# Optimization experiments

Hardware: AMD Instinct MI355X
Metric: run time of the kernel (lower is better)

Reference implementation:

```python
import jax, jax.numpy as jnp
import numpy as np
from jax import lax

# Topology constants (windowed DAG: compute node i, at global index N_IN+i,
# reads the FANIN immediately preceding global node values).
N_IN = 16      # number of input nodes
FANIN = 16     # connections per compute node
N_NODES = 512  # topologically ordered compute nodes (hidden + output)
N_OUT = 64     # last N_OUT nodes in node_order are outputs
BATCH = 32768
T = N_IN + N_NODES  # total node count


def setup_inputs() -> dict:
    key = jax.random.key(0)
    k1, k2, k3, k4 = jax.random.split(key, 4)
    x = jax.random.normal(k1, (BATCH, N_IN), dtype=jnp.float32)
    # weights scaled down so tanh is not fully saturated through 512 layers
    weights = jax.random.normal(k2, (N_NODES, FANIN), dtype=jnp.float32) * 0.25
    biases = jax.random.normal(k3, (N_NODES,), dtype=jnp.float32) * 0.1
    responses = 1.0 + 0.1 * jax.random.normal(k4, (N_NODES,), dtype=jnp.float32)
    # src indices for node i: global indices [i, i+FANIN) (== previous FANIN nodes,
    # since N_IN == FANIN). Shape [N_NODES, FANIN], int32, all in [0, T).
    src_idx = (jnp.arange(N_NODES, dtype=jnp.int32)[:, None]
               + jnp.arange(FANIN, dtype=jnp.int32)[None, :]
               + (N_IN - FANIN))
    return {"x": x, "weights": weights, "biases": biases,
            "responses": responses, "src_idx": src_idx}


def _forward(x, weights, biases, responses, src_idx):
    B = x.shape[0]
    # values buffer [B, T]: inputs first, then compute nodes in topo order
    values0 = jnp.zeros((B, T), dtype=x.dtype).at[:, :N_IN].set(x)

    def body(values, xs):
        i, idx_row, w, b, r = xs
        src_vals = jnp.take(values, idx_row, axis=1)        # [B, FANIN] gather
        agg = src_vals @ w                                   # [B] weighted sum
        out = jnp.tanh(agg + b) * r                          # activation
        values = lax.dynamic_update_slice(values, out[:, None], (0, N_IN + i))
        return values, None

    ii = jnp.arange(N_NODES, dtype=jnp.int32)
    values, _ = lax.scan(body, values0, (ii, src_idx, weights, biases, responses))
    return values[:, T - N_OUT:]  # [B, N_OUT]


def reference(x, weights, biases, responses, src_idx):
    return _forward(x, weights, biases, responses, src_idx)
```

## Files before the change

kernel.cpp:

```cpp
#include <hip/hip_runtime.h>


typedef float v4f __attribute__((ext_vector_type(4)));
typedef float v2f __attribute__((ext_vector_type(2)));

constexpr int kNOut     = 64;
constexpr int kBatch    = 32768;
constexpr int kGStrideF = 48;
constexpr int kLdsFloats = (256 + 3) * kGStrideF;
constexpr float kScale  = 2.8853900817779268f;

#define QPERM(X, CTRL) __int_as_float(__builtin_amdgcn_update_dpp(            \
    __float_as_int(X), __float_as_int(X), (CTRL), 0xF, 0xF, false))

#define PREF(S) {                                                             \
    asm volatile(                                                             \
      "ds_read_b128 %0, %5 offset:0\n\t"                                      \
      "ds_read_b128 %1, %5 offset:16\n\t"                                     \
      "ds_read_b128 %2, %5 offset:64\n\t"                                     \
      "ds_read_b128 %3, %5 offset:80\n\t"                                     \
      "ds_read_b64  %4, %5 offset:128"                                        \
      : "=&v"(qa[S]), "=&v"(qb[S]), "=&v"(qc[S]), "=&v"(qd[S]), "=&v"(qm[S])  \
      : "v"(a));                                                              \
    a += kGStrideF * 4; }

#define WAITG(S)                                                              \
    asm volatile("s_waitcnt lgkmcnt(15)"                                      \
      : "+v"(qa[S]), "+v"(qb[S]), "+v"(qc[S]), "+v"(qd[S]), "+v"(qm[S]));

#define NODE1(WLO, WHI, BH, W0,W1,W2,W3,W4,W5,W6,W7) {                        \
    float p = fmaf((W0), (WLO).x, (BH));                                      \
    p = fmaf((W1), (WLO).y, p);                                               \
    p = fmaf((W2), (WLO).z, p);                                               \
    p = fmaf((W3), (WLO).w, p);                                               \
    p = fmaf((W4), (WHI).x, p);                                               \
    p = fmaf((W5), (WHI).y, p);                                               \
    p = fmaf((W6), (WHI).z, p);                                               \
    p = fmaf((W7), (WHI).w, p);                                               \
    float sf = p + QPERM(p, 0xB1);                   \
    float ex = __builtin_amdgcn_exp2f(sf);                                    \
    float un = __builtin_amdgcn_rcpf(ex + 1.0f);                              \
    float mg = QPERM((W0), 0xB1);                      \
    (W0) = is_l1 ? un : mg; }

#define GROUP(G, O0,O1,O2,O3,O4,O5,O6,O7, P0,P1,P2,P3,P4,P5,P6,P7) {          \
    PREF(((G) + 3) & 3)                                                       \
    WAITG((G) & 3)                                                            \
    NODE1(qa[(G) & 3], qb[(G) & 3], qm[(G) & 3].x,                            \
          O0,O1,O2,O3,O4,O5,O6,O7)                                            \
    NODE1(qc[(G) & 3], qd[(G) & 3], qm[(G) & 3].y,                            \
          P0,P1,P2,P3,P4,P5,P6,P7) }

__global__ __launch_bounds__(256) void neat_fwd(
    const float* __restrict__ x,
    const float* __restrict__ w,
    const float* __restrict__ bias,
    const float* __restrict__ resp,
    float* __restrict__ out)
{
    __shared__ alignas(16) float ldsw[kLdsFloats];
    __shared__ float rst[512];
    __shared__ float sums[512];

    const int t  = threadIdx.x;
    const int jl = t & 1;
    const bool is_l1 = (jl == 1);

    rst[t] = resp[t];
    rst[t + 256] = resp[t + 256];
    __syncthreads();

    const float4* __restrict__ w4 = reinterpret_cast<const float4*>(w);
    #pragma unroll
    for (int k = 0; k < 8; ++k) {
        int i4 = t + k * 256;
        float4 v = w4[i4];
        int n = i4 >> 2, k4 = i4 & 3;
        int s0 = n + 4 * k4;
        float rho0 = (s0 + 0 < 16) ? 1.0f : rst[s0 - 16];
        float rho1 = (s0 + 1 < 16) ? 1.0f : rst[s0 - 15];
        float rho2 = (s0 + 2 < 16) ? 1.0f : rst[s0 - 14];
        float rho3 = (s0 + 3 < 16) ? 1.0f : rst[s0 - 13];
        float wr0 = v.x * rho0, wr1 = v.y * rho1,
              wr2 = v.z * rho2, wr3 = v.w * rho3;
        float ps = (wr0 + wr1) + (wr2 + wr3);
        ps += QPERM(ps, 0xB1);
        ps += QPERM(ps, 0x4E);
        if ((t & 3) == 0) sums[n] = ps;
        const float m2k = -2.0f * kScale;
        float4 sc = make_float4(wr0 * m2k, wr1 * m2k, wr2 * m2k, wr3 * m2k);
        *reinterpret_cast<float4*>(
            &ldsw[(n >> 1) * kGStrideF + (n & 1) * 16 + k4 * 4]) = sc;
    }
    __syncthreads();

    #pragma unroll
    for (int k = 0; k < 2; ++k) {
        int n = t + k * 256;
        float Bh = (bias[n] + sums[n]) * (kScale * 0.5f);
        int q = n >> 1, s = n & 1;
        ldsw[q * kGStrideF + 32 + s] = Bh;
        ldsw[q * kGStrideF + 40 + s] = Bh;
    }

    const int e = blockIdx.x * 128 + (t >> 1);
    const float4 xa = reinterpret_cast<const float4*>(x)[e * 4 + 2 * jl];
    const float4 xb = reinterpret_cast<const float4*>(x)[e * 4 + 2 * jl + 1];
    float r0 = fmaf(-0.5f, xa.x, 0.5f);
    float r1 = fmaf(-0.5f, xa.y, 0.5f);
    float r2 = fmaf(-0.5f, xa.z, 0.5f);
    float r3 = fmaf(-0.5f, xa.w, 0.5f);
    float r4 = fmaf(-0.5f, xb.x, 0.5f);
    float r5 = fmaf(-0.5f, xb.y, 0.5f);
    float r6 = fmaf(-0.5f, xb.z, 0.5f);
    float r7 = fmaf(-0.5f, xb.w, 0.5f);

    const float4* __restrict__ rr4 = reinterpret_cast<const float4*>(resp);
    float* __restrict__ op = out + (size_t)e * kNOut + jl * 8;

    __syncthreads();

    unsigned int a = (unsigned int)(unsigned long long)(&ldsw[0])
                   + (unsigned int)(jl << 5);

    v4f qa[4], qb[4], qc[4], qd[4];
    v2f qm[4];
    PREF(0) PREF(1) PREF(2)

    #pragma unroll 1
    for (int g = 0; g < 32; ++g) {
        GROUP(0, r0,r1,r2,r3,r4,r5,r6,r7,  r1,r2,r3,r4,r5,r6,r7,r0)
        GROUP(1, r2,r3,r4,r5,r6,r7,r0,r1,  r3,r4,r5,r6,r7,r0,r1,r2)
        GROUP(2, r4,r5,r6,r7,r0,r1,r2,r3,  r5,r6,r7,r0,r1,r2,r3,r4)
        GROUP(3, r6,r7,r0,r1,r2,r3,r4,r5,  r7,r0,r1,r2,r3,r4,r5,r6)
        GROUP(4, r0,r1,r2,r3,r4,r5,r6,r7,  r1,r2,r3,r4,r5,r6,r7,r0)
        GROUP(5, r2,r3,r4,r5,r6,r7,r0,r1,  r3,r4,r5,r6,r7,r0,r1,r2)
        GROUP(6, r4,r5,r6,r7,r0,r1,r2,r3,  r5,r6,r7,r0,r1,r2,r3,r4)
        GROUP(7, r6,r7,r0,r1,r2,r3,r4,r5,  r7,r0,r1,r2,r3,r4,r5,r6)
        if (g >= 28) {
            int m = g - 28;
            const float4 ra = rr4[112 + 4 * m + 2 * jl];
            const float4 rb = rr4[112 + 4 * m + 2 * jl + 1];
            float4 o0 = make_float4(fmaf(-2.0f, r0, 1.0f) * ra.x,
                                    fmaf(-2.0f, r1, 1.0f) * ra.y,
                                    fmaf(-2.0f, r2, 1.0f) * ra.z,
                                    fmaf(-2.0f, r3, 1.0f) * ra.w);
            float4 o1 = make_float4(fmaf(-2.0f, r4, 1.0f) * rb.x,
                                    fmaf(-2.0f, r5, 1.0f) * rb.y,
                                    fmaf(-2.0f, r6, 1.0f) * rb.z,
                                    fmaf(-2.0f, r7, 1.0f) * rb.w);
            *reinterpret_cast<float4*>(op + 16 * m)     = o0;
            *reinterpret_cast<float4*>(op + 16 * m + 4) = o1;
        }
    }

    asm volatile("s_waitcnt lgkmcnt(0)" ::: "memory");
}

extern "C" void kernel_launch(void* const* d_in, const int* in_sizes, int n_in,
                              void* d_out, int out_size, void* d_ws, size_t ws_size,
                              hipStream_t stream) {
    const float* x    = (const float*)d_in[0];
    const float* w    = (const float*)d_in[1];
    const float* bias = (const float*)d_in[2];
    const float* resp = (const float*)d_in[3];
    float* out = (float*)d_out;
    dim3 block(256);
    dim3 grid(kBatch / 128);
    hipLaunchKernelGGL(neat_fwd, grid, block, 0, stream, x, w, bias, resp, out);
}
```

Before: 89.35 us.

## Process two batch elements per thread pair to reuse LDS weight reads

Each thread now carries two independent batch rows (A and B) through the 512-node chain, and the block shrinks from 256 to 128 threads while still covering 128 batch rows per block. Each LDS weight/bias read now feeds twice as many FMAs, halving LDS traffic per element. The two independent dependency chains also add ILP to hide exp/rcp and DPP latency. In exchange it uses more registers per thread and fewer waves per block, which may reduce occupancy-based latency hiding.

```diff
diff --git a/kernel.cpp b/kernel.cpp
--- a/kernel.cpp
+++ b/kernel.cpp
@@ -28,30 +28,39 @@
     asm volatile("s_waitcnt lgkmcnt(15)"                                      \
       : "+v"(qa[S]), "+v"(qb[S]), "+v"(qc[S]), "+v"(qd[S]), "+v"(qm[S]));
 
-#define NODE1(WLO, WHI, BH, W0,W1,W2,W3,W4,W5,W6,W7) {                        \
-    float p = fmaf((W0), (WLO).x, (BH));                                      \
-    p = fmaf((W1), (WLO).y, p);                                               \
-    p = fmaf((W2), (WLO).z, p);                                               \
-    p = fmaf((W3), (WLO).w, p);                                               \
-    p = fmaf((W4), (WHI).x, p);                                               \
-    p = fmaf((W5), (WHI).y, p);                                               \
-    p = fmaf((W6), (WHI).z, p);                                               \
-    p = fmaf((W7), (WHI).w, p);                                               \
-    float sf = p + QPERM(p, 0xB1);                   \
-    float ex = __builtin_amdgcn_exp2f(sf);                                    \
-    float un = __builtin_amdgcn_rcpf(ex + 1.0f);                              \
-    float mg = QPERM((W0), 0xB1);                      \
-    (W0) = is_l1 ? un : mg; }
+#define NODE1(WLO, WHI, BH, A0,A1,A2,A3,A4,A5,A6,A7,                          \
+                            B0,B1,B2,B3,B4,B5,B6,B7) {                        \
+    float pA = fmaf((A0), (WLO).x, (BH));                                     \
+    float pB = fmaf((B0), (WLO).x, (BH));                                     \
+    pA = fmaf((A1), (WLO).y, pA);  pB = fmaf((B1), (WLO).y, pB);              \
+    pA = fmaf((A2), (WLO).z, pA);  pB = fmaf((B2), (WLO).z, pB);              \
+    pA = fmaf((A3), (WLO).w, pA);  pB = fmaf((B3), (WLO).w, pB);              \
+    pA = fmaf((A4), (WHI).x, pA);  pB = fmaf((B4), (WHI).x, pB);              \
+    pA = fmaf((A5), (WHI).y, pA);  pB = fmaf((B5), (WHI).y, pB);              \
+    pA = fmaf((A6), (WHI).z, pA);  pB = fmaf((B6), (WHI).z, pB);              \
+    pA = fmaf((A7), (WHI).w, pA);  pB = fmaf((B7), (WHI).w, pB);              \
+    float sA = pA + QPERM(pA, 0xB1);                 \
+    float sB = pB + QPERM(pB, 0xB1);                                          \
+    float eA_ = __builtin_amdgcn_exp2f(sA);                                   \
+    float eB_ = __builtin_amdgcn_exp2f(sB);                                   \
+    float uA = __builtin_amdgcn_rcpf(eA_ + 1.0f);                             \
+    float uB = __builtin_amdgcn_rcpf(eB_ + 1.0f);                             \
+    float mA = QPERM((A0), 0xB1);                      \
+    float mB = QPERM((B0), 0xB1);                                             \
+    (A0) = is_l1 ? uA : mA;                                                   \
+    (B0) = is_l1 ? uB : mB; }
 
 #define GROUP(G, O0,O1,O2,O3,O4,O5,O6,O7, P0,P1,P2,P3,P4,P5,P6,P7) {          \
     PREF(((G) + 3) & 3)                                                       \
     WAITG((G) & 3)                                                            \
     NODE1(qa[(G) & 3], qb[(G) & 3], qm[(G) & 3].x,                            \
-          O0,O1,O2,O3,O4,O5,O6,O7)                                            \
+          rA##O0,rA##O1,rA##O2,rA##O3,rA##O4,rA##O5,rA##O6,rA##O7,            \
+          rB##O0,rB##O1,rB##O2,rB##O3,rB##O4,rB##O5,rB##O6,rB##O7)            \
     NODE1(qc[(G) & 3], qd[(G) & 3], qm[(G) & 3].y,                            \
-          P0,P1,P2,P3,P4,P5,P6,P7) }
+          rA##P0,rA##P1,rA##P2,rA##P3,rA##P4,rA##P5,rA##P6,rA##P7,            \
+          rB##P0,rB##P1,rB##P2,rB##P3,rB##P4,rB##P5,rB##P6,rB##P7) }
 
-__global__ __launch_bounds__(256) void neat_fwd(
+__global__ __launch_bounds__(128) void neat_fwd(
     const float* __restrict__ x,
     const float* __restrict__ w,
     const float* __restrict__ bias,
@@ -66,14 +75,14 @@
     const int jl = t & 1;
     const bool is_l1 = (jl == 1);
 
-    rst[t] = resp[t];
-    rst[t + 256] = resp[t + 256];
+    #pragma unroll
+    for (int k = 0; k < 4; ++k) rst[t + k * 128] = resp[t + k * 128];
     __syncthreads();
 
     const float4* __restrict__ w4 = reinterpret_cast<const float4*>(w);
     #pragma unroll
-    for (int k = 0; k < 8; ++k) {
-        int i4 = t + k * 256;
+    for (int k = 0; k < 16; ++k) {
+        int i4 = t + k * 128;
         float4 v = w4[i4];
         int n = i4 >> 2, k4 = i4 & 3;
         int s0 = n + 4 * k4;
@@ -95,28 +104,31 @@
     __syncthreads();
 
     #pragma unroll
-    for (int k = 0; k < 2; ++k) {
-        int n = t + k * 256;
+    for (int k = 0; k < 4; ++k) {
+        int n = t + k * 128;
         float Bh = (bias[n] + sums[n]) * (kScale * 0.5f);
         int q = n >> 1, s = n & 1;
         ldsw[q * kGStrideF + 32 + s] = Bh;
         ldsw[q * kGStrideF + 40 + s] = Bh;
     }
 
-    const int e = blockIdx.x * 128 + (t >> 1);
-    const float4 xa = reinterpret_cast<const float4*>(x)[e * 4 + 2 * jl];
-    const float4 xb = reinterpret_cast<const float4*>(x)[e * 4 + 2 * jl + 1];
-    float r0 = fmaf(-0.5f, xa.x, 0.5f);
-    float r1 = fmaf(-0.5f, xa.y, 0.5f);
-    float r2 = fmaf(-0.5f, xa.z, 0.5f);
-    float r3 = fmaf(-0.5f, xa.w, 0.5f);
-    float r4 = fmaf(-0.5f, xb.x, 0.5f);
-    float r5 = fmaf(-0.5f, xb.y, 0.5f);
-    float r6 = fmaf(-0.5f, xb.z, 0.5f);
-    float r7 = fmaf(-0.5f, xb.w, 0.5f);
+    const int eA = blockIdx.x * 128 + (t >> 1);
+    const int eB = eA + 64;
+    const float4* __restrict__ x4 = reinterpret_cast<const float4*>(x);
+    const float4 xa = x4[eA * 4 + 2 * jl], xb = x4[eA * 4 + 2 * jl + 1];
+    const float4 xc = x4[eB * 4 + 2 * jl], xd = x4[eB * 4 + 2 * jl + 1];
+    float rA0 = fmaf(-0.5f, xa.x, 0.5f), rA1 = fmaf(-0.5f, xa.y, 0.5f);
+    float rA2 = fmaf(-0.5f, xa.z, 0.5f), rA3 = fmaf(-0.5f, xa.w, 0.5f);
+    float rA4 = fmaf(-0.5f, xb.x, 0.5f), rA5 = fmaf(-0.5f, xb.y, 0.5f);
+    float rA6 = fmaf(-0.5f, xb.z, 0.5f), rA7 = fmaf(-0.5f, xb.w, 0.5f);
+    float rB0 = fmaf(-0.5f, xc.x, 0.5f), rB1 = fmaf(-0.5f, xc.y, 0.5f);
+    float rB2 = fmaf(-0.5f, xc.z, 0.5f), rB3 = fmaf(-0.5f, xc.w, 0.5f);
+    float rB4 = fmaf(-0.5f, xd.x, 0.5f), rB5 = fmaf(-0.5f, xd.y, 0.5f);
+    float rB6 = fmaf(-0.5f, xd.z, 0.5f), rB7 = fmaf(-0.5f, xd.w, 0.5f);
 
     const float4* __restrict__ rr4 = reinterpret_cast<const float4*>(resp);
-    float* __restrict__ op = out + (size_t)e * kNOut + jl * 8;
+    float* __restrict__ opA = out + (size_t)eA * kNOut + jl * 8;
+    float* __restrict__ opB = out + (size_t)eB * kNOut + jl * 8;
 
     __syncthreads();
 
@@ -129,28 +141,38 @@
 
     #pragma unroll 1
     for (int g = 0; g < 32; ++g) {
-        GROUP(0, r0,r1,r2,r3,r4,r5,r6,r7,  r1,r2,r3,r4,r5,r6,r7,r0)
-        GROUP(1, r2,r3,r4,r5,r6,r7,r0,r1,  r3,r4,r5,r6,r7,r0,r1,r2)
-        GROUP(2, r4,r5,r6,r7,r0,r1,r2,r3,  r5,r6,r7,r0,r1,r2,r3,r4)
-        GROUP(3, r6,r7,r0,r1,r2,r3,r4,r5,  r7,r0,r1,r2,r3,r4,r5,r6)
-        GROUP(4, r0,r1,r2,r3,r4,r5,r6,r7,  r1,r2,r3,r4,r5,r6,r7,r0)
-        GROUP(5, r2,r3,r4,r5,r6,r7,r0,r1,  r3,r4,r5,r6,r7,r0,r1,r2)
-        GROUP(6, r4,r5,r6,r7,r0,r1,r2,r3,  r5,r6,r7,r0,r1,r2,r3,r4)
-        GROUP(7, r6,r7,r0,r1,r2,r3,r4,r5,  r7,r0,r1,r2,r3,r4,r5,r6)
+        GROUP(0, 0,1,2,3,4,5,6,7,  1,2,3,4,5,6,7,0)
+        GROUP(1, 2,3,4,5,6,7,0,1,  3,4,5,6,7,0,1,2)
+        GROUP(2, 4,5,6,7,0,1,2,3,  5,6,7,0,1,2,3,4)
+        GROUP(3, 6,7,0,1,2,3,4,5,  7,0,1,2,3,4,5,6)
+        GROUP(4, 0,1,2,3,4,5,6,7,  1,2,3,4,5,6,7,0)
+        GROUP(5, 2,3,4,5,6,7,0,1,  3,4,5,6,7,0,1,2)
+        GROUP(6, 4,5,6,7,0,1,2,3,  5,6,7,0,1,2,3,4)
+        GROUP(7, 6,7,0,1,2,3,4,5,  7,0,1,2,3,4,5,6)
         if (g >= 28) {
             int m = g - 28;
             const float4 ra = rr4[112 + 4 * m + 2 * jl];
             const float4 rb = rr4[112 + 4 * m + 2 * jl + 1];
-            float4 o0 = make_float4(fmaf(-2.0f, r0, 1.0f) * ra.x,
-                                    fmaf(-2.0f, r1, 1.0f) * ra.y,
-                                    fmaf(-2.0f, r2, 1.0f) * ra.z,
-                                    fmaf(-2.0f, r3, 1.0f) * ra.w);
-            float4 o1 = make_float4(fmaf(-2.0f, r4, 1.0f) * rb.x,
-                                    fmaf(-2.0f, r5, 1.0f) * rb.y,
-                                    fmaf(-2.0f, r6, 1.0f) * rb.z,
-                                    fmaf(-2.0f, r7, 1.0f) * rb.w);
-            *reinterpret_cast<float4*>(op + 16 * m)     = o0;
-            *reinterpret_cast<float4*>(op + 16 * m + 4) = o1;
+            float4 oA0 = make_float4(fmaf(-2.0f, rA0, 1.0f) * ra.x,
+                                     fmaf(-2.0f, rA1, 1.0f) * ra.y,
+                                     fmaf(-2.0f, rA2, 1.0f) * ra.z,
+                                     fmaf(-2.0f, rA3, 1.0f) * ra.w);
+            float4 oA1 = make_float4(fmaf(-2.0f, rA4, 1.0f) * rb.x,
+                                     fmaf(-2.0f, rA5, 1.0f) * rb.y,
+                                     fmaf(-2.0f, rA6, 1.0f) * rb.z,
+                                     fmaf(-2.0f, rA7, 1.0f) * rb.w);
+            float4 oB0 = make_float4(fmaf(-2.0f, rB0, 1.0f) * ra.x,
+                                     fmaf(-2.0f, rB1, 1.0f) * ra.y,
+                                     fmaf(-2.0f, rB2, 1.0f) * ra.z,
+                                     fmaf(-2.0f, rB3, 1.0f) * ra.w);
+            float4 oB1 = make_float4(fmaf(-2.0f, rB4, 1.0f) * rb.x,
+                                     fmaf(-2.0f, rB5, 1.0f) * rb.y,
+                                     fmaf(-2.0f, rB6, 1.0f) * rb.z,
+                                     fmaf(-2.0f, rB7, 1.0f) * rb.w);
+            *reinterpret_cast<float4*>(opA + 16 * m)     = oA0;
+            *reinterpret_cast<float4*>(opA + 16 * m + 4) = oA1;
+            *reinterpret_cast<float4*>(opB + 16 * m)     = oB0;
+            *reinterpret_cast<float4*>(opB + 16 * m + 4) = oB1;
         }
     }
 
@@ -165,7 +187,7 @@
     const float* bias = (const float*)d_in[2];
     const float* resp = (const float*)d_in[3];
     float* out = (float*)d_out;
-    dim3 block(256);
+    dim3 block(128);
     dim3 grid(kBatch / 128);
     hipLaunchKernelGGL(neat_fwd, grid, block, 0, stream, x, w, bias, resp, out);
 }
```

Result: slower. 108.5 us (+21.4%).

## Shorten node dependency chain by splitting off the newest input term

Applied to the files above, without the earlier changes.

Reworks the per-node evaluation so the most recent predecessor's contribution (weight 15) is added after the cross-lane reduction. The other 15 terms can then be computed before the previous node finishes. Each lane pair now keeps an extra register (u0/u1) holding the latest result, and the lane data layout is shifted to match. This shortens the serial critical path through the 512-node chain. In exchange the LDS reads get wider, setup has more selects, and output staging is more complex.

```diff
diff --git a/kernel.cpp b/kernel.cpp
--- a/kernel.cpp
+++ b/kernel.cpp
@@ -2,7 +2,6 @@
 
 
 typedef float v4f __attribute__((ext_vector_type(4)));
-typedef float v2f __attribute__((ext_vector_type(2)));
 
 constexpr int kNOut     = 64;
 constexpr int kBatch    = 32768;
@@ -19,7 +18,7 @@
       "ds_read_b128 %1, %5 offset:16\n\t"                                     \
       "ds_read_b128 %2, %5 offset:64\n\t"                                     \
       "ds_read_b128 %3, %5 offset:80\n\t"                                     \
-      "ds_read_b64  %4, %5 offset:128"                                        \
+      "ds_read_b128 %4, %5 offset:128"                                        \
       : "=&v"(qa[S]), "=&v"(qb[S]), "=&v"(qc[S]), "=&v"(qd[S]), "=&v"(qm[S])  \
       : "v"(a));                                                              \
     a += kGStrideF * 4; }
@@ -28,28 +27,29 @@
     asm volatile("s_waitcnt lgkmcnt(15)"                                      \
       : "+v"(qa[S]), "+v"(qb[S]), "+v"(qc[S]), "+v"(qd[S]), "+v"(qm[S]));
 
-#define NODE1(WLO, WHI, BH, W0,W1,W2,W3,W4,W5,W6,W7) {                        \
-    float p = fmaf((W0), (WLO).x, (BH));                                      \
-    p = fmaf((W1), (WLO).y, p);                                               \
-    p = fmaf((W2), (WLO).z, p);                                               \
-    p = fmaf((W3), (WLO).w, p);                                               \
-    p = fmaf((W4), (WHI).x, p);                                               \
-    p = fmaf((W5), (WHI).y, p);                                               \
-    p = fmaf((W6), (WHI).z, p);                                               \
-    p = fmaf((W7), (WHI).w, p);                                               \
-    float sf = p + QPERM(p, 0xB1);                   \
-    float ex = __builtin_amdgcn_exp2f(sf);                                    \
-    float un = __builtin_amdgcn_rcpf(ex + 1.0f);                              \
-    float mg = QPERM((W0), 0xB1);                      \
-    (W0) = is_l1 ? un : mg; }
+#define NODE1(WLO, WHI, BH, W15, UIN, UOUT, A0,A1,A2,A3,A4,A5,A6,A7) {        \
+    float p = fmaf((A0), (WLO).x, (BH));                                      \
+    p = fmaf((A1), (WLO).y, p);                                               \
+    p = fmaf((A2), (WLO).z, p);                                               \
+    p = fmaf((A3), (WLO).w, p);                                               \
+    p = fmaf((A4), (WHI).x, p);                                               \
+    p = fmaf((A5), (WHI).y, p);                                               \
+    p = fmaf((A6), (WHI).z, p);                                               \
+    p = fmaf((A7), (WHI).w, p);                                               \
+    float s_ = p + QPERM(p, 0xB1);                   \
+    float mg = QPERM((A1), 0xB1);                      \
+    float acc = fmaf((UIN), (W15), s_);                \
+    float exv = __builtin_amdgcn_exp2f(acc);                                  \
+    (UOUT) = __builtin_amdgcn_rcpf(exv + 1.0f);                               \
+    (A0) = is_l1 ? (UIN) : mg; }
 
-#define GROUP(G, O0,O1,O2,O3,O4,O5,O6,O7, P0,P1,P2,P3,P4,P5,P6,P7) {          \
+#define GROUP(G, A0,A1,A2,A3,A4,A5,A6,A7) {                                   \
     PREF(((G) + 3) & 3)                                                       \
     WAITG((G) & 3)                                                            \
-    NODE1(qa[(G) & 3], qb[(G) & 3], qm[(G) & 3].x,                            \
-          O0,O1,O2,O3,O4,O5,O6,O7)                                            \
-    NODE1(qc[(G) & 3], qd[(G) & 3], qm[(G) & 3].y,                            \
-          P0,P1,P2,P3,P4,P5,P6,P7) }
+    NODE1(qa[(G)&3], qb[(G)&3], qm[(G)&3].x, qm[(G)&3].y, u0, u1,             \
+          A0,A1,A2,A3,A4,A5,A6,A7)                                            \
+    NODE1(qc[(G)&3], qd[(G)&3], qm[(G)&3].z, qm[(G)&3].w, u1, u0,             \
+          A1,A2,A3,A4,A5,A6,A7,A0) }
 
 __global__ __launch_bounds__(256) void neat_fwd(
     const float* __restrict__ x,
@@ -60,7 +60,6 @@
 {
     __shared__ alignas(16) float ldsw[kLdsFloats];
     __shared__ float rst[512];
-    __shared__ float sums[512];
 
     const int t  = threadIdx.x;
     const int jl = t & 1;
@@ -71,49 +70,54 @@
     __syncthreads();
 
     const float4* __restrict__ w4 = reinterpret_cast<const float4*>(w);
-    #pragma unroll
-    for (int k = 0; k < 8; ++k) {
-        int i4 = t + k * 256;
-        float4 v = w4[i4];
-        int n = i4 >> 2, k4 = i4 & 3;
-        int s0 = n + 4 * k4;
-        float rho0 = (s0 + 0 < 16) ? 1.0f : rst[s0 - 16];
-        float rho1 = (s0 + 1 < 16) ? 1.0f : rst[s0 - 15];
-        float rho2 = (s0 + 2 < 16) ? 1.0f : rst[s0 - 14];
-        float rho3 = (s0 + 3 < 16) ? 1.0f : rst[s0 - 13];
-        float wr0 = v.x * rho0, wr1 = v.y * rho1,
-              wr2 = v.z * rho2, wr3 = v.w * rho3;
-        float ps = (wr0 + wr1) + (wr2 + wr3);
-        ps += QPERM(ps, 0xB1);
-        ps += QPERM(ps, 0x4E);
-        if ((t & 3) == 0) sums[n] = ps;
-        const float m2k = -2.0f * kScale;
-        float4 sc = make_float4(wr0 * m2k, wr1 * m2k, wr2 * m2k, wr3 * m2k);
-        *reinterpret_cast<float4*>(
-            &ldsw[(n >> 1) * kGStrideF + (n & 1) * 16 + k4 * 4]) = sc;
-    }
-    __syncthreads();
-
+    const float m2k = -2.0f * kScale;
     #pragma unroll
     for (int k = 0; k < 2; ++k) {
-        int n = t + k * 256;
-        float Bh = (bias[n] + sums[n]) * (kScale * 0.5f);
-        int q = n >> 1, s = n & 1;
-        ldsw[q * kGStrideF + 32 + s] = Bh;
-        ldsw[q * kGStrideF + 40 + s] = Bh;
+        int n = t + (k << 8);
+        float4 a0 = w4[n*4+0], a1 = w4[n*4+1], a2 = w4[n*4+2], a3 = w4[n*4+3];
+        float wv0=a0.x, wv1=a0.y, wv2=a0.z, wv3=a0.w;
+        float wv4=a1.x, wv5=a1.y, wv6=a1.z, wv7=a1.w;
+        float wv8=a2.x, wv9=a2.y, wv10=a2.z, wv11=a2.w;
+        float wv12=a3.x, wv13=a3.y, wv14=a3.z, wv15=a3.w;
+        float sum = 0.0f;
+        float ws0,ws1,ws2,ws3,ws4,ws5,ws6,ws7,ws8,ws9,ws10,ws11,ws12,ws13,ws14,ws15;
+        #define DO(J) { float rho = (n + J < 16) ? 1.0f : rst[n + J - 16];    \
+                        float wr = wv##J * rho; sum += wr; ws##J = wr * m2k; }
+        DO(0) DO(1) DO(2) DO(3) DO(4) DO(5) DO(6) DO(7)
+        DO(8) DO(9) DO(10) DO(11) DO(12) DO(13) DO(14) DO(15)
+        #undef DO
+        int q = n >> 1, h = n & 1;
+        float* gb = ldsw + q * kGStrideF;
+        *reinterpret_cast<float4*>(gb + h*16 + 0)  = make_float4(ws0, ws1, ws2, ws3);
+        *reinterpret_cast<float4*>(gb + h*16 + 4)  = make_float4(ws4, ws5, ws6, ws7);
+        *reinterpret_cast<float4*>(gb + h*16 + 8)  = make_float4(0.0f, ws8, ws9, ws10);
+        *reinterpret_cast<float4*>(gb + h*16 + 12) = make_float4(ws11, ws12, ws13, ws14);
+        float Bh = (bias[n] + sum) * (kScale * 0.5f);
+        gb[32 + h*2] = Bh;  gb[33 + h*2] = ws15;
+        gb[40 + h*2] = Bh;  gb[41 + h*2] = ws15;
     }
 
     const int e = blockIdx.x * 128 + (t >> 1);
-    const float4 xa = reinterpret_cast<const float4*>(x)[e * 4 + 2 * jl];
-    const float4 xb = reinterpret_cast<const float4*>(x)[e * 4 + 2 * jl + 1];
-    float r0 = fmaf(-0.5f, xa.x, 0.5f);
-    float r1 = fmaf(-0.5f, xa.y, 0.5f);
-    float r2 = fmaf(-0.5f, xa.z, 0.5f);
-    float r3 = fmaf(-0.5f, xa.w, 0.5f);
-    float r4 = fmaf(-0.5f, xb.x, 0.5f);
-    float r5 = fmaf(-0.5f, xb.y, 0.5f);
-    float r6 = fmaf(-0.5f, xb.z, 0.5f);
-    float r7 = fmaf(-0.5f, xb.w, 0.5f);
+    const float4* __restrict__ x4p = reinterpret_cast<const float4*>(x);
+    float4 X0 = x4p[e*4+0], X1 = x4p[e*4+1], X2 = x4p[e*4+2], X3 = x4p[e*4+3];
+    float xx0 = fmaf(-0.5f, X0.x, 0.5f), xx1 = fmaf(-0.5f, X0.y, 0.5f);
+    float xx2 = fmaf(-0.5f, X0.z, 0.5f), xx3 = fmaf(-0.5f, X0.w, 0.5f);
+    float xx4 = fmaf(-0.5f, X1.x, 0.5f), xx5 = fmaf(-0.5f, X1.y, 0.5f);
+    float xx6 = fmaf(-0.5f, X1.z, 0.5f), xx7 = fmaf(-0.5f, X1.w, 0.5f);
+    float xx8 = fmaf(-0.5f, X2.x, 0.5f), xx9 = fmaf(-0.5f, X2.y, 0.5f);
+    float xx10 = fmaf(-0.5f, X2.z, 0.5f), xx11 = fmaf(-0.5f, X2.w, 0.5f);
+    float xx12 = fmaf(-0.5f, X3.x, 0.5f), xx13 = fmaf(-0.5f, X3.y, 0.5f);
+    float xx14 = fmaf(-0.5f, X3.z, 0.5f), xx15 = fmaf(-0.5f, X3.w, 0.5f);
+    float r0 = is_l1 ? xx7  : xx0;
+    float r1 = is_l1 ? xx8  : xx1;
+    float r2 = is_l1 ? xx9  : xx2;
+    float r3 = is_l1 ? xx10 : xx3;
+    float r4 = is_l1 ? xx11 : xx4;
+    float r5 = is_l1 ? xx12 : xx5;
+    float r6 = is_l1 ? xx13 : xx6;
+    float r7 = is_l1 ? xx14 : xx7;
+    float u0 = xx15;
+    float u1 = 0.0f;
 
     const float4* __restrict__ rr4 = reinterpret_cast<const float4*>(resp);
     float* __restrict__ op = out + (size_t)e * kNOut + jl * 8;
@@ -123,34 +127,41 @@
     unsigned int a = (unsigned int)(unsigned long long)(&ldsw[0])
                    + (unsigned int)(jl << 5);
 
-    v4f qa[4], qb[4], qc[4], qd[4];
-    v2f qm[4];
+    v4f qa[4], qb[4], qc[4], qd[4], qm[4];
     PREF(0) PREF(1) PREF(2)
 
     #pragma unroll 1
     for (int g = 0; g < 32; ++g) {
-        GROUP(0, r0,r1,r2,r3,r4,r5,r6,r7,  r1,r2,r3,r4,r5,r6,r7,r0)
-        GROUP(1, r2,r3,r4,r5,r6,r7,r0,r1,  r3,r4,r5,r6,r7,r0,r1,r2)
-        GROUP(2, r4,r5,r6,r7,r0,r1,r2,r3,  r5,r6,r7,r0,r1,r2,r3,r4)
-        GROUP(3, r6,r7,r0,r1,r2,r3,r4,r5,  r7,r0,r1,r2,r3,r4,r5,r6)
-        GROUP(4, r0,r1,r2,r3,r4,r5,r6,r7,  r1,r2,r3,r4,r5,r6,r7,r0)
-        GROUP(5, r2,r3,r4,r5,r6,r7,r0,r1,  r3,r4,r5,r6,r7,r0,r1,r2)
-        GROUP(6, r4,r5,r6,r7,r0,r1,r2,r3,  r5,r6,r7,r0,r1,r2,r3,r4)
-        GROUP(7, r6,r7,r0,r1,r2,r3,r4,r5,  r7,r0,r1,r2,r3,r4,r5,r6)
+        GROUP(0, r0,r1,r2,r3,r4,r5,r6,r7)
+        GROUP(1, r2,r3,r4,r5,r6,r7,r0,r1)
+        GROUP(2, r4,r5,r6,r7,r0,r1,r2,r3)
+        GROUP(3, r6,r7,r0,r1,r2,r3,r4,r5)
+        GROUP(4, r0,r1,r2,r3,r4,r5,r6,r7)
+        GROUP(5, r2,r3,r4,r5,r6,r7,r0,r1)
+        GROUP(6, r4,r5,r6,r7,r0,r1,r2,r3)
+        GROUP(7, r6,r7,r0,r1,r2,r3,r4,r5)
         if (g >= 28) {
             int m = g - 28;
             const float4 ra = rr4[112 + 4 * m + 2 * jl];
             const float4 rb = rr4[112 + 4 * m + 2 * jl + 1];
-            float4 o0 = make_float4(fmaf(-2.0f, r0, 1.0f) * ra.x,
-                                    fmaf(-2.0f, r1, 1.0f) * ra.y,
-                                    fmaf(-2.0f, r2, 1.0f) * ra.z,
-                                    fmaf(-2.0f, r3, 1.0f) * ra.w);
-            float4 o1 = make_float4(fmaf(-2.0f, r4, 1.0f) * rb.x,
-                                    fmaf(-2.0f, r5, 1.0f) * rb.y,
-                                    fmaf(-2.0f, r6, 1.0f) * rb.z,
-                                    fmaf(-2.0f, r7, 1.0f) * rb.w);
-            *reinterpret_cast<float4*>(op + 16 * m)     = o0;
-            *reinterpret_cast<float4*>(op + 16 * m + 4) = o1;
+            float o0 = is_l1 ? r1 : r0;
+            float o1 = is_l1 ? r2 : r1;
+            float o2 = is_l1 ? r3 : r2;
+            float o3 = is_l1 ? r4 : r3;
+            float o4 = is_l1 ? r5 : r4;
+            float o5 = is_l1 ? r6 : r5;
+            float o6 = is_l1 ? r7 : r6;
+            float o7 = is_l1 ? u0 : r7;
+            float4 q0_ = make_float4(fmaf(-2.0f, o0, 1.0f) * ra.x,
+                                     fmaf(-2.0f, o1, 1.0f) * ra.y,
+                                     fmaf(-2.0f, o2, 1.0f) * ra.z,
+                                     fmaf(-2.0f, o3, 1.0f) * ra.w);
+            float4 q1_ = make_float4(fmaf(-2.0f, o4, 1.0f) * rb.x,
+                                     fmaf(-2.0f, o5, 1.0f) * rb.y,
+                                     fmaf(-2.0f, o6, 1.0f) * rb.z,
+                                     fmaf(-2.0f, o7, 1.0f) * rb.w);
+            *reinterpret_cast<float4*>(op + 16 * m)     = q0_;
+            *reinterpret_cast<float4*>(op + 16 * m + 4) = q1_;
         }
     }
 
```

New measurement: 89.63 us. Within noise of the previous version (+0.3%).

## Store pre-scaled weights as fp16 in LDS to halve per-node read traffic

Applied to the files above, without the earlier changes.

Folded, pre-scaled weights are now packed as fp16 pairs in LDS, so each group needs two 128-bit reads plus the bias read instead of four. The per-node LDS footprint and stride are halved, and the lgkmcnt wait threshold is adjusted to match. The weight-preparation prologue is restructured so each thread handles a whole node, which removes the cross-lane sum reduction and one barrier. The cost is an fp16-to-fp32 conversion per weight in the inner loop and reduced weight precision, which may change numerics across 512 chained nodes.

```diff
diff --git a/kernel.cpp b/kernel.cpp
--- a/kernel.cpp
+++ b/kernel.cpp
@@ -1,55 +1,61 @@
 #include <hip/hip_runtime.h>
 
 
-typedef float v4f __attribute__((ext_vector_type(4)));
-typedef float v2f __attribute__((ext_vector_type(2)));
+typedef float    v4f __attribute__((ext_vector_type(4)));
+typedef float    v2f __attribute__((ext_vector_type(2)));
+typedef _Float16 h8  __attribute__((ext_vector_type(8)));
 
-constexpr int kNOut     = 64;
-constexpr int kBatch    = 32768;
-constexpr int kGStrideF = 48;
-constexpr int kLdsFloats = (256 + 3) * kGStrideF;
-constexpr float kScale  = 2.8853900817779268f;
+constexpr int   kNOut     = 64;
+constexpr int   kBatch    = 32768;
+constexpr int   kGStrideF = 24;
+constexpr int   kGStrideB = 96;
+constexpr int   kLdsFloats = (256 + 3) * kGStrideF;
+constexpr float kScale    = 2.8853900817779268f;
 
 #define QPERM(X, CTRL) __int_as_float(__builtin_amdgcn_update_dpp(            \
     __float_as_int(X), __float_as_int(X), (CTRL), 0xF, 0xF, false))
 
+__device__ __forceinline__ unsigned pack2(float lo, float hi) {
+    _Float16 l = (_Float16)lo, h = (_Float16)hi;
+    unsigned short ul = __builtin_bit_cast(unsigned short, l);
+    unsigned short uh = __builtin_bit_cast(unsigned short, h);
+    return ((unsigned)uh << 16) | ul;
+}
+
 #define PREF(S) {                                                             \
     asm volatile(                                                             \
-      "ds_read_b128 %0, %5 offset:0\n\t"                                      \
-      "ds_read_b128 %1, %5 offset:16\n\t"                                     \
-      "ds_read_b128 %2, %5 offset:64\n\t"                                     \
-      "ds_read_b128 %3, %5 offset:80\n\t"                                     \
-      "ds_read_b64  %4, %5 offset:128"                                        \
-      : "=&v"(qa[S]), "=&v"(qb[S]), "=&v"(qc[S]), "=&v"(qd[S]), "=&v"(qm[S])  \
+      "ds_read_b128 %0, %3 offset:0\n\t"                                      \
+      "ds_read_b128 %1, %3 offset:32\n\t"                                     \
+      "ds_read_b64  %2, %3 offset:64"                                         \
+      : "=&v"(qw0[S]), "=&v"(qw1[S]), "=&v"(qm[S])                            \
       : "v"(a));                                                              \
-    a += kGStrideF * 4; }
+    a += kGStrideB; }
 
 #define WAITG(S)                                                              \
-    asm volatile("s_waitcnt lgkmcnt(15)"                                      \
-      : "+v"(qa[S]), "+v"(qb[S]), "+v"(qc[S]), "+v"(qd[S]), "+v"(qm[S]));
+    asm volatile("s_waitcnt lgkmcnt(9)"                                       \
+      : "+v"(qw0[S]), "+v"(qw1[S]), "+v"(qm[S]));
 
-#define NODE1(WLO, WHI, BH, W0,W1,W2,W3,W4,W5,W6,W7) {                        \
-    float p = fmaf((W0), (WLO).x, (BH));                                      \
-    p = fmaf((W1), (WLO).y, p);                                               \
-    p = fmaf((W2), (WLO).z, p);                                               \
-    p = fmaf((W3), (WLO).w, p);                                               \
-    p = fmaf((W4), (WHI).x, p);                                               \
-    p = fmaf((W5), (WHI).y, p);                                               \
-    p = fmaf((W6), (WHI).z, p);                                               \
-    p = fmaf((W7), (WHI).w, p);                                               \
-    float sf = p + QPERM(p, 0xB1);                   \
-    float ex = __builtin_amdgcn_exp2f(sf);                                    \
+#define NODE1(QW, BH, A0,A1,A2,A3,A4,A5,A6,A7) {                              \
+    h8 wh = __builtin_bit_cast(h8, (QW));                                     \
+    float p = fmaf((A0), (float)wh[0], (BH));                                 \
+    p = fmaf((A1), (float)wh[1], p);                                          \
+    p = fmaf((A2), (float)wh[2], p);                                          \
+    p = fmaf((A3), (float)wh[3], p);                                          \
+    p = fmaf((A4), (float)wh[4], p);                                          \
+    p = fmaf((A5), (float)wh[5], p);                                          \
+    p = fmaf((A6), (float)wh[6], p);                                          \
+    p = fmaf((A7), (float)wh[7], p);                                          \
+    float s_ = p + QPERM(p, 0xB1);                   \
+    float mg = QPERM((A0), 0xB1);                      \
+    float ex = __builtin_amdgcn_exp2f(s_);                                    \
     float un = __builtin_amdgcn_rcpf(ex + 1.0f);                              \
-    float mg = QPERM((W0), 0xB1);                      \
-    (W0) = is_l1 ? un : mg; }
+    (A0) = is_l1 ? un : mg; }
 
-#define GROUP(G, O0,O1,O2,O3,O4,O5,O6,O7, P0,P1,P2,P3,P4,P5,P6,P7) {          \
+#define GROUP(G, A0,A1,A2,A3,A4,A5,A6,A7) {                                   \
     PREF(((G) + 3) & 3)                                                       \
     WAITG((G) & 3)                                                            \
-    NODE1(qa[(G) & 3], qb[(G) & 3], qm[(G) & 3].x,                            \
-          O0,O1,O2,O3,O4,O5,O6,O7)                                            \
-    NODE1(qc[(G) & 3], qd[(G) & 3], qm[(G) & 3].y,                            \
-          P0,P1,P2,P3,P4,P5,P6,P7) }
+    NODE1(qw0[(G) & 3], qm[(G) & 3].x, A0,A1,A2,A3,A4,A5,A6,A7)               \
+    NODE1(qw1[(G) & 3], qm[(G) & 3].y, A1,A2,A3,A4,A5,A6,A7,A0) }
 
 __global__ __launch_bounds__(256) void neat_fwd(
     const float* __restrict__ x,
@@ -60,7 +66,6 @@
 {
     __shared__ alignas(16) float ldsw[kLdsFloats];
     __shared__ float rst[512];
-    __shared__ float sums[512];
 
     const int t  = threadIdx.x;
     const int jl = t & 1;
@@ -71,41 +76,37 @@
     __syncthreads();
 
     const float4* __restrict__ w4 = reinterpret_cast<const float4*>(w);
-    #pragma unroll
-    for (int k = 0; k < 8; ++k) {
-        int i4 = t + k * 256;
-        float4 v = w4[i4];
-        int n = i4 >> 2, k4 = i4 & 3;
-        int s0 = n + 4 * k4;
-        float rho0 = (s0 + 0 < 16) ? 1.0f : rst[s0 - 16];
-        float rho1 = (s0 + 1 < 16) ? 1.0f : rst[s0 - 15];
-        float rho2 = (s0 + 2 < 16) ? 1.0f : rst[s0 - 14];
-        float rho3 = (s0 + 3 < 16) ? 1.0f : rst[s0 - 13];
-        float wr0 = v.x * rho0, wr1 = v.y * rho1,
-              wr2 = v.z * rho2, wr3 = v.w * rho3;
-        float ps = (wr0 + wr1) + (wr2 + wr3);
-        ps += QPERM(ps, 0xB1);
-        ps += QPERM(ps, 0x4E);
-        if ((t & 3) == 0) sums[n] = ps;
-        const float m2k = -2.0f * kScale;
-        float4 sc = make_float4(wr0 * m2k, wr1 * m2k, wr2 * m2k, wr3 * m2k);
-        *reinterpret_cast<float4*>(
-            &ldsw[(n >> 1) * kGStrideF + (n & 1) * 16 + k4 * 4]) = sc;
-    }
-    __syncthreads();
-
+    const float m2k = -2.0f * kScale;
     #pragma unroll
     for (int k = 0; k < 2; ++k) {
-        int n = t + k * 256;
-        float Bh = (bias[n] + sums[n]) * (kScale * 0.5f);
-        int q = n >> 1, s = n & 1;
-        ldsw[q * kGStrideF + 32 + s] = Bh;
-        ldsw[q * kGStrideF + 40 + s] = Bh;
+        int n = t + (k << 8);
+        const float4* wn = w4 + n * 4;
+        float4 a0 = wn[0], a1 = wn[1], a2 = wn[2], a3 = wn[3];
+        float sum = 0.0f;
+        float ws0,ws1,ws2,ws3,ws4,ws5,ws6,ws7,ws8,ws9,ws10,ws11,ws12,ws13,ws14,ws15;
+        #define DO(J, V) { float rho = (n + (J) < 16) ? 1.0f : rst[n + (J) - 16]; \
+                           float wr = (V) * rho; sum += wr; ws##J = wr * m2k; }
+        DO(0,a0.x)  DO(1,a0.y)  DO(2,a0.z)  DO(3,a0.w)
+        DO(4,a1.x)  DO(5,a1.y)  DO(6,a1.z)  DO(7,a1.w)
+        DO(8,a2.x)  DO(9,a2.y)  DO(10,a2.z) DO(11,a2.w)
+        DO(12,a3.x) DO(13,a3.y) DO(14,a3.z) DO(15,a3.w)
+        #undef DO
+        int q = n >> 1, h = n & 1;
+        uint4 lo = make_uint4(pack2(ws0,ws1),  pack2(ws2,ws3),
+                              pack2(ws4,ws5),  pack2(ws6,ws7));
+        uint4 hi = make_uint4(pack2(ws8,ws9),  pack2(ws10,ws11),
+                              pack2(ws12,ws13), pack2(ws14,ws15));
+        uint4* dst = reinterpret_cast<uint4*>(&ldsw[q * kGStrideF + h * 8]);
+        dst[0] = lo;
+        dst[1] = hi;
+        float Bh = (bias[n] + sum) * (kScale * 0.5f);
+        ldsw[q * kGStrideF + 16 + h] = Bh;
+        ldsw[q * kGStrideF + 20 + h] = Bh;
     }
 
     const int e = blockIdx.x * 128 + (t >> 1);
-    const float4 xa = reinterpret_cast<const float4*>(x)[e * 4 + 2 * jl];
-    const float4 xb = reinterpret_cast<const float4*>(x)[e * 4 + 2 * jl + 1];
+    const float4* __restrict__ x4p = reinterpret_cast<const float4*>(x);
+    const float4 xa = x4p[e * 4 + 2 * jl], xb = x4p[e * 4 + 2 * jl + 1];
     float r0 = fmaf(-0.5f, xa.x, 0.5f);
     float r1 = fmaf(-0.5f, xa.y, 0.5f);
     float r2 = fmaf(-0.5f, xa.z, 0.5f);
@@ -121,22 +122,22 @@
     __syncthreads();
 
     unsigned int a = (unsigned int)(unsigned long long)(&ldsw[0])
-                   + (unsigned int)(jl << 5);
+                   + (unsigned int)(jl << 4);
 
-    v4f qa[4], qb[4], qc[4], qd[4];
+    v4f qw0[4], qw1[4];
     v2f qm[4];
     PREF(0) PREF(1) PREF(2)
 
     #pragma unroll 1
     for (int g = 0; g < 32; ++g) {
-        GROUP(0, r0,r1,r2,r3,r4,r5,r6,r7,  r1,r2,r3,r4,r5,r6,r7,r0)
-        GROUP(1, r2,r3,r4,r5,r6,r7,r0,r1,  r3,r4,r5,r6,r7,r0,r1,r2)
-        GROUP(2, r4,r5,r6,r7,r0,r1,r2,r3,  r5,r6,r7,r0,r1,r2,r3,r4)
-        GROUP(3, r6,r7,r0,r1,r2,r3,r4,r5,  r7,r0,r1,r2,r3,r4,r5,r6)
-        GROUP(4, r0,r1,r2,r3,r4,r5,r6,r7,  r1,r2,r3,r4,r5,r6,r7,r0)
-        GROUP(5, r2,r3,r4,r5,r6,r7,r0,r1,  r3,r4,r5,r6,r7,r0,r1,r2)
-        GROUP(6, r4,r5,r6,r7,r0,r1,r2,r3,  r5,r6,r7,r0,r1,r2,r3,r4)
-        GROUP(7, r6,r7,r0,r1,r2,r3,r4,r5,  r7,r0,r1,r2,r3,r4,r5,r6)
+        GROUP(0, r0,r1,r2,r3,r4,r5,r6,r7)
+        GROUP(1, r2,r3,r4,r5,r6,r7,r0,r1)
+        GROUP(2, r4,r5,r6,r7,r0,r1,r2,r3)
+        GROUP(3, r6,r7,r0,r1,r2,r3,r4,r5)
+        GROUP(4, r0,r1,r2,r3,r4,r5,r6,r7)
+        GROUP(5, r2,r3,r4,r5,r6,r7,r0,r1)
+        GROUP(6, r4,r5,r6,r7,r0,r1,r2,r3)
+        GROUP(7, r6,r7,r0,r1,r2,r3,r4,r5)
         if (g >= 28) {
             int m = g - 28;
             const float4 ra = rr4[112 + 4 * m + 2 * jl];
```

Measured after the change: 88.64 us. About the same (-0.8%).
